# Performance work log

Measured on AMD Instinct MI355X. Metric: run time of the kernel, lower is better.

The kernel has to match this reference:

```python
import jax, jax.numpy as jnp
import numpy as np
from jax import lax

B, C, H, T = 128, 64, 32, 256


def _xavier(key, shape):
    fan_out, fan_in = shape[-2], shape[-1]
    s = np.sqrt(6.0 / (fan_in + fan_out)).astype(np.float32)
    return jax.random.uniform(key, shape, jnp.float32, -s, s)


def setup_inputs() -> dict:
    key = jax.random.key(0)
    ks = jax.random.split(key, 12)
    x = jax.random.normal(ks[0], (B, C, T), jnp.float32)
    m = jax.random.uniform(ks[1], (B, C, T), jnp.float32)
    d = jax.random.uniform(ks[2], (B, C, T), jnp.float32)
    Wf = _xavier(ks[3], (C, H, H))
    Vf = _xavier(ks[4], (C, H, 3))
    cf = _xavier(ks[5], (C, H, 1))[:, :, 0]          # (C, H)
    Wb = _xavier(ks[6], (C, H, H))
    Vb = _xavier(ks[7], (C, H, 3))
    cb = _xavier(ks[8], (C, H, 1))[:, :, 0]          # (C, H)
    U = _xavier(ks[9], (C, 1, 2 * H))[:, 0, :]        # (C, 2H)
    c0 = 0.1 * jax.random.normal(ks[10], (C,), jnp.float32)
    return {"x": x, "m": m, "d": d, "Wf": Wf, "Vf": Vf, "cf": cf,
            "Wb": Wb, "Vb": Vb, "cb": cb, "U": U, "c0": c0}


def _mrnn(x, m, d, Wf, Vf, cf, Wb, Vb, cb, U, c0):
    act = jax.nn.relu
    Tn = x.shape[-1]
    pad = lambda a: jnp.pad(a, ((0, 0), (0, 0), (1, 1)), mode="edge")  # replication pad
    feats = jnp.stack([pad(x), pad(m), pad(d)], axis=-1)   # (B, C, T+2, 3)
    # forward RNN sees padded times 0..T-1 (orig t-1); backward sees padded T+1..2 (orig t+1)
    in_f = jnp.transpose(feats[:, :, :Tn], (2, 0, 1, 3))               # (T, B, C, 3)
    in_b = jnp.transpose(feats[:, :, 2:Tn + 2][:, :, ::-1], (2, 0, 1, 3))

    def scan_rnn(W, V, c, inp):
        def step(h, v):
            # per-channel block-diagonal matmul: batched tiny GEMM over C
            hn = act(jnp.einsum("chk,bck->bch", W, h)
                     + jnp.einsum("chj,bcj->bch", V, v) + c)
            return hn, hn
        h0 = jnp.zeros((x.shape[0], W.shape[0], W.shape[1]), x.dtype)
        return lax.scan(step, h0, inp)[1]                  # (T, B, C, H)

    hf = scan_rnn(Wf, Vf, cf, in_f)
    hb = scan_rnn(Wb, Vb, cb, in_b)[::-1]                  # align backward states with t
    hcat = jnp.concatenate([hf, hb], axis=-1)              # (T, B, C, 2H)
    out = act(jnp.einsum("ck,tbck->tbc", U, hcat) + c0)    # (T, B, C)
    return jnp.transpose(out, (1, 2, 0))                   # (B, C, T)


def reference(x, m, d, Wf, Vf, cf, Wb, Vb, cb, U, c0):
    return _mrnn(x, m, d, Wf, Vf, cf, Wb, Vb, cb, U, c0)
```

## Files before the change

### kernel.cpp

```cpp
#include <hip/hip_runtime.h>

constexpr int Bn = 128, Cn = 64, Hn = 32, Tn = 256;

typedef __attribute__((ext_vector_type(8))) short short8;
typedef __attribute__((ext_vector_type(4))) float f32x4;

__device__ __forceinline__ void split_bf16(float f, short& hi, short& lo) {
  unsigned u = __float_as_uint(f);
  hi = (short)(u >> 16);
  float r = f - __uint_as_float(u & 0xffff0000u);
  lo = (short)(__float_as_uint(r) >> 16);
}

__global__ __launch_bounds__(64)
void mrnn_scan(const float* __restrict__ x, const float* __restrict__ m,
               const float* __restrict__ d,
               const float* __restrict__ Wf, const float* __restrict__ Vf,
               const float* __restrict__ cf,
               const float* __restrict__ Wb, const float* __restrict__ Vb,
               const float* __restrict__ cb,
               const float* __restrict__ U,
               float* __restrict__ pf_out, float* __restrict__ pb_out) {
  const int bid = blockIdx.x;
  const int dir = bid >> 9;
  const int c   = (bid >> 3) & (Cn - 1);
  const int g   = bid & 7;
  const int tid = threadIdx.x;
  const int q = tid >> 4;
  const int n = tid & 15;
  const int b = g * 16 + n;

  const float* W  = dir ? Wb : Wf;
  const float* V  = dir ? Vb : Vf;
  const float* cc = dir ? cb : cf;

  const int ra0 = 8 * (n >> 2) + (n & 3);
  const int ra1 = ra0 + 4;
  short8 A0h, A0l, A1h, A1l;
#pragma unroll
  for (int j = 0; j < 8; ++j) {
    const float w0 = W[(c * Hn + ra0) * Hn + 8 * q + j];
    const float w1 = W[(c * Hn + ra1) * Hn + 8 * q + j];
    short hi, lo;
    split_bf16(w0, hi, lo); A0h[j] = hi; A0l[j] = lo;
    split_bf16(w1, hi, lo); A1h[j] = hi; A1l[j] = lo;
  }

  float v0x[4], v0y[4], v0z[4], bs0[4], uu0[4];
  float v1x[4], v1y[4], v1z[4], bs1[4], uu1[4];
#pragma unroll
  for (int r = 0; r < 4; ++r) {
    const int row0 = 8 * q + r, row1 = row0 + 4;
    const float* vp0 = V + (c * Hn + row0) * 3;
    v0x[r] = vp0[0]; v0y[r] = vp0[1]; v0z[r] = vp0[2];
    bs0[r] = cc[c * Hn + row0];
    uu0[r] = U[c * 2 * Hn + dir * Hn + row0];
    const float* vp1 = V + (c * Hn + row1) * 3;
    v1x[r] = vp1[0]; v1y[r] = vp1[1]; v1z[r] = vp1[2];
    bs1[r] = cc[c * Hn + row1];
    uu1[r] = U[c * 2 * Hn + dir * Hn + row1];
  }

  short8 Bh = {0, 0, 0, 0, 0, 0, 0, 0};
  short8 Bl = {0, 0, 0, 0, 0, 0, 0, 0};

  const long base = ((long)b * Cn + c) * Tn;
  const float* px = x + base;
  const float* pm = m + base;
  const float* pd = d + base;
  float* pout = (dir ? pb_out : pf_out) + base;

  float cx, cm2, cd2;
  f32x4 qx, qm, qd;
  if (!dir) {
    cx = px[0]; cm2 = pm[0]; cd2 = pd[0];
    qx = *(const f32x4*)px; qm = *(const f32x4*)pm; qd = *(const f32x4*)pd;
  } else {
    cx = px[Tn - 1]; cm2 = pm[Tn - 1]; cd2 = pd[Tn - 1];
    qx = *(const f32x4*)(px + Tn - 4);
    qm = *(const f32x4*)(pm + Tn - 4);
    qd = *(const f32x4*)(pd + Tn - 4);
  }

  for (int t0 = 0; t0 < Tn; t0 += 4) {
    int qn_ = dir ? (Tn - 8 - t0) : (t0 + 4);
    if (qn_ < 0) qn_ = 0;
    if (qn_ > Tn - 4) qn_ = Tn - 4;
    const f32x4 nqx = *(const f32x4*)(px + qn_);
    const f32x4 nqm = *(const f32x4*)(pm + qn_);
    const f32x4 nqd = *(const f32x4*)(pd + qn_);

    float inx[4], inm[4], ind[4];
    if (!dir) {
      inx[0] = cx;  inx[1] = qx.x; inx[2] = qx.y; inx[3] = qx.z; cx  = qx.w;
      inm[0] = cm2; inm[1] = qm.x; inm[2] = qm.y; inm[3] = qm.z; cm2 = qm.w;
      ind[0] = cd2; ind[1] = qd.x; ind[2] = qd.y; ind[3] = qd.z; cd2 = qd.w;
    } else {
      inx[0] = cx;  inx[1] = qx.w; inx[2] = qx.z; inx[3] = qx.y; cx  = qx.x;
      inm[0] = cm2; inm[1] = qm.w; inm[2] = qm.z; inm[3] = qm.y; cm2 = qm.x;
      ind[0] = cd2; ind[1] = qd.w; ind[2] = qd.z; ind[3] = qd.y; cd2 = qd.x;
    }

    f32x4 pacc;
#pragma unroll
    for (int u = 0; u < 4; ++u) {
      const float ix = inx[u], im = inm[u], idv = ind[u];
      f32x4 acc0, acc1;
#pragma unroll
      for (int r = 0; r < 4; ++r) {
        acc0[r] = fmaf(v0x[r], ix, fmaf(v0y[r], im, fmaf(v0z[r], idv, bs0[r])));
        acc1[r] = fmaf(v1x[r], ix, fmaf(v1y[r], im, fmaf(v1z[r], idv, bs1[r])));
      }
      acc0 = __builtin_amdgcn_mfma_f32_16x16x32_bf16(A0l, Bh, acc0, 0, 0, 0);
      acc1 = __builtin_amdgcn_mfma_f32_16x16x32_bf16(A1l, Bh, acc1, 0, 0, 0);
      acc0 = __builtin_amdgcn_mfma_f32_16x16x32_bf16(A0h, Bl, acc0, 0, 0, 0);
      acc1 = __builtin_amdgcn_mfma_f32_16x16x32_bf16(A1h, Bl, acc1, 0, 0, 0);
      acc0 = __builtin_amdgcn_mfma_f32_16x16x32_bf16(A0h, Bh, acc0, 0, 0, 0);
      acc1 = __builtin_amdgcn_mfma_f32_16x16x32_bf16(A1h, Bh, acc1, 0, 0, 0);
#pragma unroll
      for (int r = 0; r < 4; ++r) {
        acc0[r] = fmaxf(acc0[r], 0.f);
        acc1[r] = fmaxf(acc1[r], 0.f);
      }
      float p = uu0[0] * acc0[0];
      p = fmaf(uu0[1], acc0[1], p); p = fmaf(uu0[2], acc0[2], p);
      p = fmaf(uu0[3], acc0[3], p);
      p = fmaf(uu1[0], acc1[0], p); p = fmaf(uu1[1], acc1[1], p);
      p = fmaf(uu1[2], acc1[2], p); p = fmaf(uu1[3], acc1[3], p);
      p += __shfl_xor(p, 16);
      p += __shfl_xor(p, 32);
      pacc[dir ? (3 - u) : u] = p;
#pragma unroll
      for (int r = 0; r < 4; ++r) {
        short hi, lo;
        split_bf16(acc0[r], hi, lo); Bh[r] = hi;     Bl[r] = lo;
        split_bf16(acc1[r], hi, lo); Bh[4 + r] = hi; Bl[4 + r] = lo;
      }
    }
    if (q == 0) {
      if (!dir) *(f32x4*)(pout + t0) = pacc;
      else      *(f32x4*)(pout + (Tn - 4 - t0)) = pacc;
    }
    qx = nqx; qm = nqm; qd = nqd;
  }
}

__global__ __launch_bounds__(256)
void mrnn_combine(const float* __restrict__ pb, const float* __restrict__ c0,
                  float* __restrict__ out) {
  const int i4 = blockIdx.x * 256 + threadIdx.x;
  const int c = (i4 >> 6) & (Cn - 1);
  const float c0v = c0[c];
  float4 a = ((const float4*)out)[i4];
  const float4 bb = ((const float4*)pb)[i4];
  a.x = fmaxf(a.x + bb.x + c0v, 0.f);
  a.y = fmaxf(a.y + bb.y + c0v, 0.f);
  a.z = fmaxf(a.z + bb.z + c0v, 0.f);
  a.w = fmaxf(a.w + bb.w + c0v, 0.f);
  ((float4*)out)[i4] = a;
}

extern "C" void kernel_launch(void* const* d_in, const int* in_sizes, int n_in,
                              void* d_out, int out_size, void* d_ws, size_t ws_size,
                              hipStream_t stream) {
  const float* x  = (const float*)d_in[0];
  const float* m  = (const float*)d_in[1];
  const float* dd = (const float*)d_in[2];
  const float* Wf = (const float*)d_in[3];
  const float* Vf = (const float*)d_in[4];
  const float* cf = (const float*)d_in[5];
  const float* Wb = (const float*)d_in[6];
  const float* Vb = (const float*)d_in[7];
  const float* cb = (const float*)d_in[8];
  const float* U  = (const float*)d_in[9];
  const float* c0 = (const float*)d_in[10];
  float* out = (float*)d_out;
  float* pb  = (float*)d_ws;

  mrnn_scan<<<1024, 64, 0, stream>>>(x, m, dd, Wf, Vf, cf, Wb, Vb, cb, U, out, pb);
  mrnn_combine<<<(Bn * Cn * Tn) / (256 * 4), 256, 0, stream>>>(pb, c0, out);
}
```

Before: 165.9 us.

## Fuse forward/backward scans and combine into one kernel via shared memory

Each block now runs both directions as two wavefronts, keeps per-timestep projections in LDS, and applies the combine (sum, bias, relu) in-kernel, dropping the second launch and the global workspace round trip. The MFMA chain is restructured so the low-part products accumulate into a separate zero-initialized accumulator, which shortens the dependent MFMA chain per step. Bf16 packing of the hidden state uses v_perm byte permutes, and the low part is rounded instead of truncated. Block count halves to 512 with 128 threads, which changes occupancy and latency hiding of the serial recurrence.

Result: slower. 207.9 us (+25.3%).

```diff
diff --git a/kernel.cpp b/kernel.cpp
--- a/kernel.cpp
+++ b/kernel.cpp
@@ -4,31 +4,40 @@
 
 typedef __attribute__((ext_vector_type(8))) short short8;
 typedef __attribute__((ext_vector_type(4))) float f32x4;
+typedef __attribute__((ext_vector_type(4))) unsigned int u32x4;
 
-__device__ __forceinline__ void split_bf16(float f, short& hi, short& lo) {
-  unsigned u = __float_as_uint(f);
-  hi = (short)(u >> 16);
-  float r = f - __uint_as_float(u & 0xffff0000u);
-  lo = (short)(__float_as_uint(r) >> 16);
+__device__ __forceinline__ unsigned pk_hi(unsigned y, unsigned x) {
+  return __builtin_amdgcn_perm(y, x, 0x07060302u);
 }
 
-__global__ __launch_bounds__(64)
-void mrnn_scan(const float* __restrict__ x, const float* __restrict__ m,
-               const float* __restrict__ d,
-               const float* __restrict__ Wf, const float* __restrict__ Vf,
-               const float* __restrict__ cf,
-               const float* __restrict__ Wb, const float* __restrict__ Vb,
-               const float* __restrict__ cb,
-               const float* __restrict__ U,
-               float* __restrict__ pf_out, float* __restrict__ pb_out) {
+__device__ __forceinline__ void wsplit(float w, short& hi, short& lo) {
+  unsigned u = __float_as_uint(w);
+  float r = w - __uint_as_float(u & 0xffff0000u);
+  unsigned ru = __float_as_uint(r) + 0x8000u;
+  hi = (short)(u >> 16);
+  lo = (short)(ru >> 16);
+}
+
+__global__ __launch_bounds__(128)
+void mrnn_fused(const float* __restrict__ x, const float* __restrict__ m,
+                const float* __restrict__ d,
+                const float* __restrict__ Wf, const float* __restrict__ Vf,
+                const float* __restrict__ cf,
+                const float* __restrict__ Wb, const float* __restrict__ Vb,
+                const float* __restrict__ cb,
+                const float* __restrict__ U, const float* __restrict__ c0,
+                float* __restrict__ out) {
   const int bid = blockIdx.x;
-  const int dir = bid >> 9;
-  const int c   = (bid >> 3) & (Cn - 1);
+  const int c   = bid >> 3;
   const int g   = bid & 7;
   const int tid = threadIdx.x;
-  const int q = tid >> 4;
-  const int n = tid & 15;
+  const int dir  = tid >> 6;
+  const int lane = tid & 63;
+  const int q = lane >> 4;
+  const int n = lane & 15;
   const int b = g * 16 + n;
+
+  __shared__ __align__(16) float pbuf[2][16][260];
 
   const float* W  = dir ? Wb : Wf;
   const float* V  = dir ? Vb : Vf;
@@ -39,11 +48,9 @@
   short8 A0h, A0l, A1h, A1l;
 #pragma unroll
   for (int j = 0; j < 8; ++j) {
-    const float w0 = W[(c * Hn + ra0) * Hn + 8 * q + j];
-    const float w1 = W[(c * Hn + ra1) * Hn + 8 * q + j];
     short hi, lo;
-    split_bf16(w0, hi, lo); A0h[j] = hi; A0l[j] = lo;
-    split_bf16(w1, hi, lo); A1h[j] = hi; A1l[j] = lo;
+    wsplit(W[(c * Hn + ra0) * Hn + 8 * q + j], hi, lo); A0h[j] = hi; A0l[j] = lo;
+    wsplit(W[(c * Hn + ra1) * Hn + 8 * q + j], hi, lo); A1h[j] = hi; A1l[j] = lo;
   }
 
   float v0x[4], v0y[4], v0z[4], bs0[4], uu0[4];
@@ -61,14 +68,14 @@
     uu1[r] = U[c * 2 * Hn + dir * Hn + row1];
   }
 
-  short8 Bh = {0, 0, 0, 0, 0, 0, 0, 0};
-  short8 Bl = {0, 0, 0, 0, 0, 0, 0, 0};
+  u32x4 Bh = {0u, 0u, 0u, 0u};
+  u32x4 Bl = {0u, 0u, 0u, 0u};
+  const f32x4 z4 = {0.f, 0.f, 0.f, 0.f};
 
   const long base = ((long)b * Cn + c) * Tn;
   const float* px = x + base;
   const float* pm = m + base;
   const float* pd = d + base;
-  float* pout = (dir ? pb_out : pf_out) + base;
 
   float cx, cm2, cd2;
   f32x4 qx, qm, qd;
@@ -105,59 +112,70 @@
 #pragma unroll
     for (int u = 0; u < 4; ++u) {
       const float ix = inx[u], im = inm[u], idv = ind[u];
-      f32x4 acc0, acc1;
+      f32x4 vi0, vi1;
 #pragma unroll
       for (int r = 0; r < 4; ++r) {
-        acc0[r] = fmaf(v0x[r], ix, fmaf(v0y[r], im, fmaf(v0z[r], idv, bs0[r])));
-        acc1[r] = fmaf(v1x[r], ix, fmaf(v1y[r], im, fmaf(v1z[r], idv, bs1[r])));
+        vi0[r] = fmaf(v0x[r], ix, fmaf(v0y[r], im, fmaf(v0z[r], idv, bs0[r])));
+        vi1[r] = fmaf(v1x[r], ix, fmaf(v1y[r], im, fmaf(v1z[r], idv, bs1[r])));
       }
-      acc0 = __builtin_amdgcn_mfma_f32_16x16x32_bf16(A0l, Bh, acc0, 0, 0, 0);
-      acc1 = __builtin_amdgcn_mfma_f32_16x16x32_bf16(A1l, Bh, acc1, 0, 0, 0);
-      acc0 = __builtin_amdgcn_mfma_f32_16x16x32_bf16(A0h, Bl, acc0, 0, 0, 0);
-      acc1 = __builtin_amdgcn_mfma_f32_16x16x32_bf16(A1h, Bl, acc1, 0, 0, 0);
-      acc0 = __builtin_amdgcn_mfma_f32_16x16x32_bf16(A0h, Bh, acc0, 0, 0, 0);
-      acc1 = __builtin_amdgcn_mfma_f32_16x16x32_bf16(A1h, Bh, acc1, 0, 0, 0);
+      const short8 bh = __builtin_bit_cast(short8, Bh);
+      const short8 bl = __builtin_bit_cast(short8, Bl);
+      f32x4 s0 = __builtin_amdgcn_mfma_f32_16x16x32_bf16(A0l, bh, z4, 0, 0, 0);
+      f32x4 s1 = __builtin_amdgcn_mfma_f32_16x16x32_bf16(A1l, bh, z4, 0, 0, 0);
+      f32x4 a0 = __builtin_amdgcn_mfma_f32_16x16x32_bf16(A0h, bh, vi0, 0, 0, 0);
+      f32x4 a1 = __builtin_amdgcn_mfma_f32_16x16x32_bf16(A1h, bh, vi1, 0, 0, 0);
+      s0 = __builtin_amdgcn_mfma_f32_16x16x32_bf16(A0h, bl, s0, 0, 0, 0);
+      s1 = __builtin_amdgcn_mfma_f32_16x16x32_bf16(A1h, bl, s1, 0, 0, 0);
+      f32x4 h0, h1;
 #pragma unroll
       for (int r = 0; r < 4; ++r) {
-        acc0[r] = fmaxf(acc0[r], 0.f);
-        acc1[r] = fmaxf(acc1[r], 0.f);
+        h0[r] = fmaxf(a0[r] + s0[r], 0.f);
+        h1[r] = fmaxf(a1[r] + s1[r], 0.f);
       }
-      float p = uu0[0] * acc0[0];
-      p = fmaf(uu0[1], acc0[1], p); p = fmaf(uu0[2], acc0[2], p);
-      p = fmaf(uu0[3], acc0[3], p);
-      p = fmaf(uu1[0], acc1[0], p); p = fmaf(uu1[1], acc1[1], p);
-      p = fmaf(uu1[2], acc1[2], p); p = fmaf(uu1[3], acc1[3], p);
+      float p = uu0[0] * h0[0];
+      p = fmaf(uu0[1], h0[1], p); p = fmaf(uu0[2], h0[2], p);
+      p = fmaf(uu0[3], h0[3], p);
+      p = fmaf(uu1[0], h1[0], p); p = fmaf(uu1[1], h1[1], p);
+      p = fmaf(uu1[2], h1[2], p); p = fmaf(uu1[3], h1[3], p);
       p += __shfl_xor(p, 16);
       p += __shfl_xor(p, 32);
       pacc[dir ? (3 - u) : u] = p;
+      const unsigned h00 = __float_as_uint(h0[0]), h01 = __float_as_uint(h0[1]);
+      const unsigned h02 = __float_as_uint(h0[2]), h03 = __float_as_uint(h0[3]);
+      const unsigned h10 = __float_as_uint(h1[0]), h11 = __float_as_uint(h1[1]);
+      const unsigned h12 = __float_as_uint(h1[2]), h13 = __float_as_uint(h1[3]);
+      Bh[0] = pk_hi(h01, h00); Bh[1] = pk_hi(h03, h02);
+      Bh[2] = pk_hi(h11, h10); Bh[3] = pk_hi(h13, h12);
+      unsigned ru[8];
 #pragma unroll
       for (int r = 0; r < 4; ++r) {
-        short hi, lo;
-        split_bf16(acc0[r], hi, lo); Bh[r] = hi;     Bl[r] = lo;
-        split_bf16(acc1[r], hi, lo); Bh[4 + r] = hi; Bl[4 + r] = lo;
+        ru[r]     = __float_as_uint(h0[r] - __uint_as_float(__float_as_uint(h0[r]) & 0xffff0000u)) + 0x8000u;
+        ru[4 + r] = __float_as_uint(h1[r] - __uint_as_float(__float_as_uint(h1[r]) & 0xffff0000u)) + 0x8000u;
       }
+      Bl[0] = pk_hi(ru[1], ru[0]); Bl[1] = pk_hi(ru[3], ru[2]);
+      Bl[2] = pk_hi(ru[5], ru[4]); Bl[3] = pk_hi(ru[7], ru[6]);
     }
     if (q == 0) {
-      if (!dir) *(f32x4*)(pout + t0) = pacc;
-      else      *(f32x4*)(pout + (Tn - 4 - t0)) = pacc;
+      float* dst = &pbuf[dir][n][dir ? (Tn - 4 - t0) : t0];
+      *(f32x4*)dst = pacc;
     }
     qx = nqx; qm = nqm; qd = nqd;
   }
-}
 
-__global__ __launch_bounds__(256)
-void mrnn_combine(const float* __restrict__ pb, const float* __restrict__ c0,
-                  float* __restrict__ out) {
-  const int i4 = blockIdx.x * 256 + threadIdx.x;
-  const int c = (i4 >> 6) & (Cn - 1);
+  __syncthreads();
+
   const float c0v = c0[c];
-  float4 a = ((const float4*)out)[i4];
-  const float4 bb = ((const float4*)pb)[i4];
-  a.x = fmaxf(a.x + bb.x + c0v, 0.f);
-  a.y = fmaxf(a.y + bb.y + c0v, 0.f);
-  a.z = fmaxf(a.z + bb.z + c0v, 0.f);
-  a.w = fmaxf(a.w + bb.w + c0v, 0.f);
-  ((float4*)out)[i4] = a;
+#pragma unroll
+  for (int i = 0; i < 8; ++i) {
+    const int nn = 2 * i + (tid >> 6);
+    const int tt = (tid & 63) << 2;
+    const f32x4 pf  = *(const f32x4*)&pbuf[0][nn][tt];
+    const f32x4 pbv = *(const f32x4*)&pbuf[1][nn][tt];
+    f32x4 o;
+#pragma unroll
+    for (int e = 0; e < 4; ++e) o[e] = fmaxf(pf[e] + pbv[e] + c0v, 0.f);
+    *(f32x4*)(out + (((long)((g * 16 + nn) * Cn + c)) << 8) + tt) = o;
+  }
 }
 
 extern "C" void kernel_launch(void* const* d_in, const int* in_sizes, int n_in,
@@ -175,8 +193,6 @@
   const float* U  = (const float*)d_in[9];
   const float* c0 = (const float*)d_in[10];
   float* out = (float*)d_out;
-  float* pb  = (float*)d_ws;
 
-  mrnn_scan<<<1024, 64, 0, stream>>>(x, m, dd, Wf, Vf, cf, Wb, Vb, cb, U, out, pb);
-  mrnn_combine<<<(Bn * Cn * Tn) / (256 * 4), 256, 0, stream>>>(pb, c0, out);
+  mrnn_fused<<<512, 128, 0, stream>>>(x, m, dd, Wf, Vf, cf, Wb, Vb, cb, U, c0, out);
 }
```
